# Kernel optimization log

Hardware: AMD Instinct MI355X
Metric: run time of the kernel (lower is better)

## Reference

```python
import jax, jax.numpy as jnp
import numpy as np

DIM = 1024
NUM_HEADS = 16
HEAD_DIM = 64
EPS = 1e-6

def setup_inputs() -> dict:
    key = jax.random.key(0)
    ks = jax.random.split(key, 6)
    x = jax.random.normal(ks[0], (4, 2048, DIM), dtype=jnp.float32)
    # Linear weights stored as (in, out); torch nn.Linear computes x @ W.T with W (out,in),
    # equivalent math with our (in,out) layout.
    Wq = jax.random.normal(ks[1], (DIM, NUM_HEADS * HEAD_DIM), dtype=jnp.float32) / np.sqrt(DIM)
    Wk = jax.random.normal(ks[2], (DIM, NUM_HEADS * HEAD_DIM), dtype=jnp.float32) / np.sqrt(DIM)
    Wv = jax.random.normal(ks[3], (DIM, NUM_HEADS * HEAD_DIM), dtype=jnp.float32) / np.sqrt(DIM)
    Wo = jax.random.normal(ks[4], (NUM_HEADS * HEAD_DIM, DIM), dtype=jnp.float32) / np.sqrt(NUM_HEADS * HEAD_DIM)
    # FeatureMap buffer: randn(head_dim, head_dim)/sqrt(head_dim)
    proj = jax.random.normal(ks[5], (HEAD_DIM, HEAD_DIM), dtype=jnp.float32) / np.sqrt(HEAD_DIM)
    return {"x": x, "Wq": Wq, "Wk": Wk, "Wv": Wv, "Wo": Wo, "proj": proj}

def _feature_map(x, proj):
    # phi(x) = elu(x @ proj) + 1  (positive features)
    return jax.nn.elu(x @ proj) + 1.0

def reference(x, Wq, Wk, Wv, Wo, proj):
    B, S, _ = x.shape
    H, D = NUM_HEADS, HEAD_DIM
    q = (x @ Wq).reshape(B, S, H, D)
    k = (x @ Wk).reshape(B, S, H, D)
    v = (x @ Wv).reshape(B, S, H, D)
    q = _feature_map(q, proj)
    k = _feature_map(k, proj)
    # scan over time: carry kv_state (B,H,D,D) and k_state (B,H,D)
    q_t = jnp.moveaxis(q, 1, 0)  # (S,B,H,D)
    k_t = jnp.moveaxis(k, 1, 0)
    v_t = jnp.moveaxis(v, 1, 0)

    def step(carry, qkv):
        kv, ksum = carry
        qt, kt, vt = qkv  # each (B,H,D)
        kv = kv + kt[..., :, None] * vt[..., None, :]  # outer product k v^T
        ksum = ksum + kt
        num = jnp.einsum('bhd,bhde->bhe', qt, kv)
        den = jnp.einsum('bhd,bhd->bh', qt, ksum) + EPS
        return (kv, ksum), num / den[..., None]

    kv0 = jnp.zeros((B, H, D, D), dtype=x.dtype)
    ks0 = jnp.zeros((B, H, D), dtype=x.dtype)
    _, out = jax.lax.scan(step, (kv0, ks0), (q_t, k_t, v_t))
    out = jnp.moveaxis(out, 0, 1).reshape(B, S, H * D)  # (B,S,H*D)
    return out @ Wo
```

## Files before the change

kernel.cpp:

```cpp
#include <hip/hip_runtime.h>

typedef unsigned short u16;
typedef unsigned int   u32;
typedef short bfrag8 __attribute__((ext_vector_type(8)));
typedef float facc4  __attribute__((ext_vector_type(4)));

#define DIM    1024
#define NH     16
#define HD     64
#define BSZ    4
#define SEQ    2048
#define MROWS  (BSZ*SEQ)
#define CHUNK  64
#define NCHUNK (SEQ/CHUNK)
#define BH     (BSZ*NH)
#define TS     72
#define NT32   32

__device__ __forceinline__ u16 f2bf(float f) {
  u32 u = __builtin_bit_cast(u32, f);
  u32 r = u + 0x7fffu + ((u >> 16) & 1u);
  return (u16)(r >> 16);
}
__device__ __forceinline__ float bf2f(u16 b) {
  return __builtin_bit_cast(float, (u32)b << 16);
}

__device__ __forceinline__ void gload_lds16(const void* g, void* l) {
  __builtin_amdgcn_global_load_lds((const __attribute__((address_space(1))) u32*)g,
                                   (__attribute__((address_space(3))) u32*)l, 16, 0, 0);
}


__global__ __launch_bounds__(256) void conv_f32_bf16(const float* __restrict__ in, u16* __restrict__ out) {
  const int i = (blockIdx.x * 256 + threadIdx.x) * 4;
  const float4 v = *(const float4*)(in + i);
  ushort4 o;
  o.x = f2bf(v.x); o.y = f2bf(v.y); o.z = f2bf(v.z); o.w = f2bf(v.w);
  *(ushort4*)(out + i) = o;
}

__global__ __launch_bounds__(256) void fold_qk(const float* __restrict__ Wq, const float* __restrict__ Wk,
                                               const float* __restrict__ proj, u16* __restrict__ wt) {
  const int i0 = blockIdx.x * 32;
  const int h  = blockIdx.y;
  const int sel = blockIdx.z;
  const float* W = sel ? Wk : Wq;
  u16* out = wt + (size_t)sel * (DIM*DIM);
  __shared__ float sp[64*64];
  __shared__ float sw[32*64];
  const int tid = threadIdx.x;
  for (int idx = tid; idx < 4096; idx += 256) sp[idx] = proj[idx];
  for (int idx = tid; idx < 2048; idx += 256) {
    int r = idx >> 6, c = idx & 63;
    sw[idx] = W[(size_t)(i0 + r)*DIM + h*64 + c];
  }
  __syncthreads();
  const int i  = tid >> 3;
  const int e0 = (tid & 7) * 8;
  #pragma unroll
  for (int ee = 0; ee < 8; ++ee) {
    const int e = e0 + ee;
    float acc = 0.f;
    for (int d = 0; d < 64; ++d) acc += sw[i*64 + d] * sp[d*64 + e];
    out[(size_t)(h*64 + e)*DIM + i0 + i] = f2bf(acc);
  }
}

__global__ __launch_bounds__(256) void trans_conv(const float* __restrict__ Wv, const float* __restrict__ Wo,
                                                  u16* __restrict__ wt) {
  const int sel = blockIdx.z;
  const float* in = sel ? Wo : Wv;
  u16* out = wt + (size_t)(2 + sel) * (DIM*DIM);
  const int n0 = blockIdx.x * 32, k0 = blockIdx.y * 32;
  __shared__ float tile[32][33];
  const int tid = threadIdx.x;
  for (int idx = tid; idx < 1024; idx += 256) {
    int r = idx >> 5, c = idx & 31;
    tile[r][c] = in[(size_t)(k0 + r)*DIM + n0 + c];
  }
  __syncthreads();
  for (int idx = tid; idx < 1024; idx += 256) {
    int r = idx >> 5, c = idx & 31;
    out[(size_t)(n0 + r)*DIM + k0 + c] = f2bf(tile[c][r]);
  }
}

template<int MODE>
__global__ __launch_bounds__(256, 3)
void gemm128(const u16* __restrict__ A, const u16* __restrict__ W,
             u16* __restrict__ outb, float* __restrict__ outf) {
  __shared__ u16 lds[2][2][4096];
  const int tid  = threadIdx.x;
  const int wave = tid >> 6, lane = tid & 63;
  const int wm = wave >> 1, wn = wave & 1;
  const int lr = lane & 15, g = lane >> 4;

  const int NY  = (MODE == 0) ? 24 : 8;
  const int q   = (int)gridDim.x >> 3;
  const int bid = (int)blockIdx.x;
  const int nf_ = (bid & 7) * q + (bid >> 3);
  const int m0  = (nf_ / NY) * 128;
  const int ngl = (nf_ % NY) * 128;

  auto stage = [&](int kt) {
    #pragma unroll
    for (int o = 0; o < 2; ++o) {
      const int L = o*256 + tid;
      const int row = L >> 2, s = L & 3;
      const int gc = ((s ^ ((row >> 1) & 3)) << 3);
      gload_lds16(A + (size_t)(m0  + row)*DIM + kt*32 + gc, &lds[kt & 1][0][(o*256 + wave*64)*8]);
      gload_lds16(W + (size_t)(ngl + row)*DIM + kt*32 + gc, &lds[kt & 1][1][(o*256 + wave*64)*8]);
    }
  };

  stage(0);
  __syncthreads();

  facc4 acc[4][4] = {};

  for (int t = 0; t < NT32; ++t) {
    if (t + 1 < NT32) stage(t + 1);
    const u16* lX = &lds[t & 1][0][0];
    const u16* lW = &lds[t & 1][1][0];
    bfrag8 xf[4], wf[4];
    #pragma unroll
    for (int mf = 0; mf < 4; ++mf) {
      const int row = wm*64 + mf*16 + lr;
      xf[mf] = *(const bfrag8*)&lX[row*32 + ((g ^ ((row >> 1) & 3)) << 3)];
    }
    #pragma unroll
    for (int nf = 0; nf < 4; ++nf) {
      const int row = wn*64 + nf*16 + lr;
      wf[nf] = *(const bfrag8*)&lW[row*32 + ((g ^ ((row >> 1) & 3)) << 3)];
    }
    __builtin_amdgcn_s_setprio(1);
    #pragma unroll
    for (int nf = 0; nf < 4; ++nf)
      #pragma unroll
      for (int mf = 0; mf < 4; ++mf)
        acc[nf][mf] = __builtin_amdgcn_mfma_f32_16x16x32_bf16(wf[nf], xf[mf], acc[nf][mf], 0, 0, 0);
    __builtin_amdgcn_s_setprio(0);
    __syncthreads();
  }

  const int sel = (MODE == 0) ? (ngl >> 10) : 0;
  const bool doElu = (MODE == 0) && (sel < 2);
  const int coly = (MODE == 0) ? (ngl & 1023) : ngl;
  #pragma unroll
  for (int nf = 0; nf < 4; ++nf) {
    #pragma unroll
    for (int mf = 0; mf < 4; ++mf) {
      const facc4 a = acc[nf][mf];
      const int m = m0 + wm*64 + mf*16 + lr;
      const int col0 = coly + wn*64 + nf*16 + g*4;
      float v0 = a[0], v1 = a[1], v2 = a[2], v3 = a[3];
      if (MODE == 0) {
        if (doElu) {
          v0 = (v0 > 0.f) ? (v0 + 1.f) : __expf(v0);
          v1 = (v1 > 0.f) ? (v1 + 1.f) : __expf(v1);
          v2 = (v2 > 0.f) ? (v2 + 1.f) : __expf(v2);
          v3 = (v3 > 0.f) ? (v3 + 1.f) : __expf(v3);
        }
        uint2 pk;
        pk.x = (u32)f2bf(v0) | ((u32)f2bf(v1) << 16);
        pk.y = (u32)f2bf(v2) | ((u32)f2bf(v3) << 16);
        *(uint2*)&outb[(size_t)sel*((size_t)MROWS*DIM) + (size_t)m*DIM + col0] = pk;
      } else {
        float4 pk; pk.x = v0; pk.y = v1; pk.z = v2; pk.w = v3;
        *(float4*)&outf[(size_t)m*DIM + col0] = pk;
      }
    }
  }
}


__global__ __launch_bounds__(256) void phaseA(const u16* __restrict__ Kb, const u16* __restrict__ Vb,
                                              u16* __restrict__ Ast, float* __restrict__ ksum) {
  const int c = blockIdx.x, bh = blockIdx.y;
  const int b = bh >> 4, h = bh & 15;
  const int tid = threadIdx.x;
  const int wave = tid >> 6, lane = tid & 63, lr = lane & 15, g = lane >> 4;
  __shared__ u16 lKt[64*TS];
  __shared__ u16 lVt[64*TS];
  const size_t mbase = (size_t)b*SEQ + (size_t)c*CHUNK;

  for (int s = tid; s < 512; s += 256) {
    const int t = s >> 3, dg = (s & 7) * 8;
    const bfrag8 kk = *(const bfrag8*)&Kb[(mbase + t)*DIM + h*64 + dg];
    const bfrag8 vv = *(const bfrag8*)&Vb[(mbase + t)*DIM + h*64 + dg];
    #pragma unroll
    for (int j = 0; j < 8; ++j) {
      lKt[(dg + j)*TS + t] = (u16)kk[j];
      lVt[(dg + j)*TS + t] = (u16)vv[j];
    }
  }
  __syncthreads();

  facc4 acc[4] = {};
  #pragma unroll
  for (int kt = 0; kt < 2; ++kt) {
    const bfrag8 af = *(const bfrag8*)&lVt[(wave*16 + lr)*TS + kt*32 + g*8];
    #pragma unroll
    for (int j = 0; j < 4; ++j) {
      const bfrag8 bk = *(const bfrag8*)&lKt[(j*16 + lr)*TS + kt*32 + g*8];
      acc[j] = __builtin_amdgcn_mfma_f32_16x16x32_bf16(af, bk, acc[j], 0, 0, 0);
    }
  }
  u16* dst = Ast + (((size_t)bh*NCHUNK + c) << 12);
  #pragma unroll
  for (int j = 0; j < 4; ++j)
    #pragma unroll
    for (int r = 0; r < 4; ++r)
      dst[(wave*16 + g*4 + r)*64 + j*16 + lr] = f2bf(acc[j][r]);

  const int d = tid >> 2, seg = tid & 3;
  const bfrag8 k0 = *(const bfrag8*)&lKt[d*TS + seg*16];
  const bfrag8 k1 = *(const bfrag8*)&lKt[d*TS + seg*16 + 8];
  float s = 0.f;
  #pragma unroll
  for (int j = 0; j < 8; ++j) s += bf2f((u16)k0[j]) + bf2f((u16)k1[j]);
  s += __shfl_xor(s, 1, 64);
  s += __shfl_xor(s, 2, 64);
  if (seg == 0) ksum[((size_t)bh*NCHUNK + c)*64 + d] = s;
}

__global__ __launch_bounds__(256) void phaseB(u16* __restrict__ Ast, float* __restrict__ ksum) {
  const int bh = blockIdx.x, slice = blockIdx.y;
  const int tid = threadIdx.x;
  u16* base = Ast + (size_t)bh*NCHUNK*4096 + slice*256 + tid;
  float v[NCHUNK];
  #pragma unroll
  for (int c = 0; c < NCHUNK; ++c) v[c] = bf2f(base[(size_t)c*4096]);
  float run = 0.f;
  #pragma unroll
  for (int c = 0; c < NCHUNK; ++c) { base[(size_t)c*4096] = f2bf(run); run += v[c]; }
  if (slice == 0 && tid < 64) {
    float rs = 0.f;
    float* kp = ksum + (size_t)bh*NCHUNK*64 + tid;
    for (int c = 0; c < NCHUNK; ++c) { const float t = kp[c*64]; kp[c*64] = rs; rs += t; }
  }
}

__global__ __launch_bounds__(256) void phaseC(const u16* __restrict__ Qb, const u16* __restrict__ Kb,
                                              const u16* __restrict__ Vb, const u16* __restrict__ Ast,
                                              const float* __restrict__ ksum, u16* __restrict__ Ob) {
  const int c = blockIdx.x, bh = blockIdx.y;
  const int b = bh >> 4, h = bh & 15;
  const int tid = threadIdx.x;
  const int wave = tid >> 6, lane = tid & 63, lr = lane & 15, g = lane >> 4;
  __shared__ u16 lS  [64*TS];
  __shared__ u16 lVt [64*TS];
  __shared__ u16 lKVt[64*TS];
  __shared__ float lks[64];
  __shared__ float lrs[64];
  __shared__ float lqk[64];
  const size_t mbase = (size_t)b*SEQ + (size_t)c*CHUNK;

  for (int s = tid; s < 512; s += 256) {
    const int t = s >> 3, dg = (s & 7) * 8;
    const bfrag8 vv = *(const bfrag8*)&Vb[(mbase + t)*DIM + h*64 + dg];
    #pragma unroll
    for (int j = 0; j < 8; ++j) lVt[(dg + j)*TS + t] = (u16)vv[j];
  }
  const u16* kvsrc = Ast + (((size_t)bh*NCHUNK + c) << 12);
  for (int s = tid; s < 512; s += 256) {
    const int e = s >> 3, dg = (s & 7) * 8;
    *(bfrag8*)&lKVt[e*TS + dg] = *(const bfrag8*)&kvsrc[e*64 + dg];
  }
  if (tid < 64) lks[tid] = ksum[((size_t)bh*NCHUNK + c)*64 + tid];

  bfrag8 qf[2], kf[4][2];
  {
    const u16* qrow = Qb + (mbase + wave*16 + lr)*DIM + h*64;
    qf[0] = *(const bfrag8*)&qrow[g*8];
    qf[1] = *(const bfrag8*)&qrow[32 + g*8];
  }
  #pragma unroll
  for (int j = 0; j < 4; ++j) {
    const u16* krow = Kb + (mbase + j*16 + lr)*DIM + h*64;
    kf[j][0] = *(const bfrag8*)&krow[g*8];
    kf[j][1] = *(const bfrag8*)&krow[32 + g*8];
  }

  facc4 accs[4] = {};
  #pragma unroll
  for (int kt = 0; kt < 2; ++kt)
    #pragma unroll
    for (int j = 0; j < 4; ++j)
      accs[j] = __builtin_amdgcn_mfma_f32_16x16x32_bf16(qf[kt], kf[j][kt], accs[j], 0, 0, 0);

  float rs[4] = {0.f, 0.f, 0.f, 0.f};
  #pragma unroll
  for (int j = 0; j < 4; ++j) {
    const int cc = j*16 + lr;
    #pragma unroll
    for (int r = 0; r < 4; ++r) {
      const int rr = wave*16 + g*4 + r;
      const float vS = (cc <= rr) ? accs[j][r] : 0.f;
      rs[r] += vS;
      lS[rr*TS + cc] = f2bf(vS);
    }
  }
  #pragma unroll
  for (int r = 0; r < 4; ++r) {
    float t = rs[r];
    t += __shfl_xor(t, 1, 64); t += __shfl_xor(t, 2, 64);
    t += __shfl_xor(t, 4, 64); t += __shfl_xor(t, 8, 64);
    if (lr == 0) lrs[wave*16 + g*4 + r] = t;
  }
  __syncthreads();

  {
    const u16* qr2 = Qb + (mbase + wave*16 + lr)*DIM + h*64 + g*16;
    const bfrag8 a0 = *(const bfrag8*)&qr2[0];
    const bfrag8 a1 = *(const bfrag8*)&qr2[8];
    float t = 0.f;
    #pragma unroll
    for (int j = 0; j < 8; ++j)
      t += bf2f((u16)a0[j]) * lks[g*16 + j] + bf2f((u16)a1[j]) * lks[g*16 + 8 + j];
    t += __shfl_xor(t, 16, 64);
    t += __shfl_xor(t, 32, 64);
    if (g == 0) lqk[wave*16 + lr] = t;
  }

  facc4 acco[4] = {};
  #pragma unroll
  for (int kt = 0; kt < 2; ++kt) {
    const bfrag8 sf = *(const bfrag8*)&lS[(wave*16 + lr)*TS + kt*32 + g*8];
    #pragma unroll
    for (int j = 0; j < 4; ++j) {
      const bfrag8 vf = *(const bfrag8*)&lVt[(j*16 + lr)*TS + kt*32 + g*8];
      acco[j] = __builtin_amdgcn_mfma_f32_16x16x32_bf16(sf, vf, acco[j], 0, 0, 0);
    }
  }
  #pragma unroll
  for (int kt = 0; kt < 2; ++kt)
    #pragma unroll
    for (int j = 0; j < 4; ++j) {
      const bfrag8 kvf = *(const bfrag8*)&lKVt[(j*16 + lr)*TS + kt*32 + g*8];
      acco[j] = __builtin_amdgcn_mfma_f32_16x16x32_bf16(qf[kt], kvf, acco[j], 0, 0, 0);
    }

  #pragma unroll
  for (int r = 0; r < 4; ++r) {
    const int rr = wave*16 + g*4 + r;
    const float rden = 1.0f / (lrs[rr] + lqk[rr] + 1e-6f);
    #pragma unroll
    for (int j = 0; j < 4; ++j)
      Ob[(mbase + rr)*DIM + h*64 + j*16 + lr] = f2bf(acco[j][r] * rden);
  }
}

extern "C" void kernel_launch(void* const* d_in, const int* in_sizes, int n_in,
                              void* d_out, int out_size, void* d_ws, size_t ws_size,
                              hipStream_t stream) {
  const float* x    = (const float*)d_in[0];
  const float* Wq   = (const float*)d_in[1];
  const float* Wk   = (const float*)d_in[2];
  const float* Wv   = (const float*)d_in[3];
  const float* Wo   = (const float*)d_in[4];
  const float* proj = (const float*)d_in[5];
  float* out = (float*)d_out;

  char* ws = (char*)d_ws;
  u16*   xb   = (u16*)  (ws);
  u16*   wt   = (u16*)  (ws + 16777216);
  u16*   qkv  = (u16*)  (ws + 25165824);
  u16*   Ob   = (u16*)  (ws + 75497472);
  u16*   Ast  = (u16*)  (ws + 92274688);
  float* ksum = (float*)(ws + 109051904);
  (void)ws_size; (void)in_sizes; (void)n_in; (void)out_size;

  conv_f32_bf16<<<dim3((MROWS*DIM)/1024), 256, 0, stream>>>(x, xb);
  fold_qk      <<<dim3(DIM/32, NH, 2), 256, 0, stream>>>(Wq, Wk, proj, wt);
  trans_conv   <<<dim3(DIM/32, DIM/32, 2), 256, 0, stream>>>(Wv, Wo, wt);

  gemm128<0><<<dim3(64*24), 256, 0, stream>>>(xb, wt, qkv, nullptr);

  const u16* Qb = qkv;
  const u16* Kb = qkv + (size_t)MROWS*DIM;
  const u16* Vb = qkv + 2*(size_t)MROWS*DIM;

  phaseA<<<dim3(NCHUNK, BH), 256, 0, stream>>>(Kb, Vb, Ast, ksum);
  phaseB<<<dim3(BH, 16), 256, 0, stream>>>(Ast, ksum);
  phaseC<<<dim3(NCHUNK, BH), 256, 0, stream>>>(Qb, Kb, Vb, Ast, ksum, Ob);

  gemm128<1><<<dim3(64*8), 256, 0, stream>>>(Ob, wt + 3*(size_t)DIM*DIM, nullptr, out);
}
```

Before: 192.7 us.

## Rewrite GEMMs as 128x256 tiles with triple-buffered LDS and phased MFMA schedule

Replaces the 128x128, 256-thread, double-buffered GEMM with a 512-thread kernel that computes 128x256 output tiles using a K-step of 64 and three LDS buffers. The loop is split into explicit phases, each with barriers, priority raises and vmcnt waits, so global-to-LDS loads for later K-steps interleave with MFMA clusters and fragment reads are register double-buffered. The aim is to raise data reuse per tile and hide load latency behind MFMA work. The cost is a large LDS footprint that allows one block per CU, fewer blocks for the output GEMM (256), and fragile hand-tuned waitcnt accounting.

```diff
diff --git a/kernel.cpp b/kernel.cpp
--- a/kernel.cpp
+++ b/kernel.cpp
@@ -15,7 +15,7 @@
 #define NCHUNK (SEQ/CHUNK)
 #define BH     (BSZ*NH)
 #define TS     72
-#define NT32   32
+#define NT     16
 
 __device__ __forceinline__ u16 f2bf(float f) {
   u32 u = __builtin_bit_cast(u32, f);
@@ -86,89 +86,149 @@
   }
 }
 
+
+#define PH_OPEN() { asm volatile("s_barrier" ::: "memory"); __builtin_amdgcn_sched_barrier(0); \
+                    __builtin_amdgcn_s_setprio(1); }
+#define PH_CLOSE(VM) { __builtin_amdgcn_s_setprio(0); __builtin_amdgcn_sched_barrier(0); \
+                       asm volatile("s_waitcnt vmcnt(" #VM ")" ::: "memory"); \
+                       asm volatile("s_barrier" ::: "memory"); }
+#define PH_CLOSE0() { __builtin_amdgcn_s_setprio(0); __builtin_amdgcn_sched_barrier(0); \
+                      asm volatile("s_barrier" ::: "memory"); }
+
+#define SU(mat, rb, kt, dstbase, seg) \
+  gload_lds16((mat) + (size_t)((rb) + (seg)*64 + (tid>>3))*DIM + (kt)*64 + ((((tid)&7) ^ ((tid>>3)&7)) << 3), \
+              (dstbase) + (seg)*4096 + tid*8);
+
+#define RDX01(dst, XB) { _Pragma("unroll") for(int mf=0;mf<2;++mf){ _Pragma("unroll") for(int kh=0;kh<2;++kh){ \
+  const int row = wm*64 + mf*16 + lr; \
+  dst[mf*2+kh] = *(const bfrag8*)&(XB)[row*64 + (((kh*4+g) ^ (row&7)) << 3)]; } } }
+#define RDX23(dst, XB) { _Pragma("unroll") for(int mf=0;mf<2;++mf){ _Pragma("unroll") for(int kh=0;kh<2;++kh){ \
+  const int row = wm*64 + (2+mf)*16 + lr; \
+  dst[mf*2+kh] = *(const bfrag8*)&(XB)[row*64 + (((kh*4+g) ^ (row&7)) << 3)]; } } }
+#define RDW01(dst, WB) { _Pragma("unroll") for(int nf=0;nf<2;++nf){ _Pragma("unroll") for(int kh=0;kh<2;++kh){ \
+  const int row = wn*32 + nf*16 + lr; \
+  dst[nf*2+kh] = *(const bfrag8*)&(WB)[row*64 + (((kh*4+g) ^ (row&7)) << 3)]; } } }
+#define RDW23(dst, WB) { _Pragma("unroll") for(int nf=0;nf<2;++nf){ _Pragma("unroll") for(int kh=0;kh<2;++kh){ \
+  const int row = 128 + wn*32 + nf*16 + lr; \
+  dst[nf*2+kh] = *(const bfrag8*)&(WB)[row*64 + (((kh*4+g) ^ (row&7)) << 3)]; } } }
+
+#define MMQ(NHh, MHh, XF, WF) { \
+  _Pragma("unroll") for(int nf=0;nf<2;++nf){ _Pragma("unroll") for(int mf=0;mf<2;++mf){ \
+  _Pragma("unroll") for(int kh=0;kh<2;++kh){ \
+    acc[(NHh)*2+nf][(MHh)*2+mf] = __builtin_amdgcn_mfma_f32_16x16x32_bf16( \
+        WF[nf*2+kh], XF[mf*2+kh], acc[(NHh)*2+nf][(MHh)*2+mf], 0, 0, 0); } } } }
+
 template<int MODE>
-__global__ __launch_bounds__(256, 3)
-void gemm128(const u16* __restrict__ A, const u16* __restrict__ W,
-             u16* __restrict__ outb, float* __restrict__ outf) {
-  __shared__ u16 lds[2][2][4096];
+__global__ __launch_bounds__(512, 1)
+void gemmR(const u16* __restrict__ A, const u16* __restrict__ W,
+           u16* __restrict__ outb, float* __restrict__ outf) {
+  __shared__ u16 lds[3*8192 + 3*16384];
+  u16* ldsX = lds;
+  u16* ldsW = lds + 3*8192;
   const int tid  = threadIdx.x;
   const int wave = tid >> 6, lane = tid & 63;
-  const int wm = wave >> 1, wn = wave & 1;
+  const int wm = wave >> 2, wn = wave & 3;
   const int lr = lane & 15, g = lane >> 4;
 
-  const int NY  = (MODE == 0) ? 24 : 8;
+  const int NY  = (MODE == 0) ? 12 : 4;
   const int q   = (int)gridDim.x >> 3;
   const int bid = (int)blockIdx.x;
   const int nf_ = (bid & 7) * q + (bid >> 3);
   const int m0  = (nf_ / NY) * 128;
-  const int ngl = (nf_ % NY) * 128;
-
-  auto stage = [&](int kt) {
-    #pragma unroll
-    for (int o = 0; o < 2; ++o) {
-      const int L = o*256 + tid;
-      const int row = L >> 2, s = L & 3;
-      const int gc = ((s ^ ((row >> 1) & 3)) << 3);
-      gload_lds16(A + (size_t)(m0  + row)*DIM + kt*32 + gc, &lds[kt & 1][0][(o*256 + wave*64)*8]);
-      gload_lds16(W + (size_t)(ngl + row)*DIM + kt*32 + gc, &lds[kt & 1][1][(o*256 + wave*64)*8]);
-    }
-  };
-
-  stage(0);
-  __syncthreads();
+  const int ngl = (nf_ % NY) * 256;
+
+  SU(A, m0, 0, ldsX, 0);            SU(A, m0, 0, ldsX, 1);
+  SU(W, ngl, 0, ldsW, 0);           SU(W, ngl, 0, ldsW, 1);
+  SU(W, ngl, 0, ldsW, 2);           SU(W, ngl, 0, ldsW, 3);
+  SU(A, m0, 1, ldsX + 8192, 0);     SU(A, m0, 1, ldsX + 8192, 1);
+  SU(W, ngl, 1, ldsW + 16384, 0);   SU(W, ngl, 1, ldsW + 16384, 1);
+  SU(W, ngl, 1, ldsW + 16384, 2);   SU(W, ngl, 1, ldsW + 16384, 3);
+  asm volatile("s_waitcnt vmcnt(6)" ::: "memory");
+  asm volatile("s_barrier" ::: "memory");
 
   facc4 acc[4][4] = {};
-
-  for (int t = 0; t < NT32; ++t) {
-    if (t + 1 < NT32) stage(t + 1);
-    const u16* lX = &lds[t & 1][0][0];
-    const u16* lW = &lds[t & 1][1][0];
-    bfrag8 xf[4], wf[4];
-    #pragma unroll
-    for (int mf = 0; mf < 4; ++mf) {
-      const int row = wm*64 + mf*16 + lr;
-      xf[mf] = *(const bfrag8*)&lX[row*32 + ((g ^ ((row >> 1) & 3)) << 3)];
-    }
-    #pragma unroll
-    for (int nf = 0; nf < 4; ++nf) {
-      const int row = wn*64 + nf*16 + lr;
-      wf[nf] = *(const bfrag8*)&lW[row*32 + ((g ^ ((row >> 1) & 3)) << 3)];
-    }
-    __builtin_amdgcn_s_setprio(1);
-    #pragma unroll
-    for (int nf = 0; nf < 4; ++nf)
-      #pragma unroll
-      for (int mf = 0; mf < 4; ++mf)
-        acc[nf][mf] = __builtin_amdgcn_mfma_f32_16x16x32_bf16(wf[nf], xf[mf], acc[nf][mf], 0, 0, 0);
+  bfrag8 xf01a[4], xf23a[4], wf01a[4], wf23a[4];
+  bfrag8 xf01b[4], xf23b[4], wf01b[4], wf23b[4];
+
+  RDX01(xf01a, ldsX); RDW01(wf01a, ldsW);
+
+  int bE = 0, bO = 1, bS = 2;
+  for (int p = 0; p < 7; ++p) {
+    const int E = 2*p;
+    const u16* xbE = ldsX + bE*8192;   u16* xbEm = ldsX + bE*8192;
+    const u16* wbE = ldsW + bE*16384;  u16* wbEm = ldsW + bE*16384;
+    const u16* xbO = ldsX + bO*8192;
+    const u16* wbO = ldsW + bO*16384;
+    u16* xbS = ldsX + bS*8192;
+    u16* wbS = ldsW + bS*16384;
+    RDX23(xf23a, xbE); SU(A, m0, E+2, xbS, 0); SU(A, m0, E+2, xbS, 1);
+    PH_OPEN(); MMQ(0,0,xf01a,wf01a); PH_CLOSE(8);
+    RDW23(wf23a, wbE); SU(W, ngl, E+2, wbS, 0); SU(W, ngl, E+2, wbS, 1);
+    PH_OPEN(); MMQ(0,1,xf23a,wf01a); PH_CLOSE(8);
+    RDX01(xf01b, xbO); SU(W, ngl, E+2, wbS, 2); SU(W, ngl, E+2, wbS, 3);
+    PH_OPEN(); MMQ(1,0,xf01a,wf23a); PH_CLOSE(8);
+    RDW01(wf01b, wbO);
+    PH_OPEN(); MMQ(1,1,xf23a,wf23a); PH_CLOSE0();
+    RDX23(xf23b, xbO); SU(A, m0, E+3, xbEm, 0); SU(A, m0, E+3, xbEm, 1);
+    PH_OPEN(); MMQ(0,0,xf01b,wf01b); PH_CLOSE(8);
+    RDW23(wf23b, wbO); SU(W, ngl, E+3, wbEm, 0); SU(W, ngl, E+3, wbEm, 1);
+    PH_OPEN(); MMQ(0,1,xf23b,wf01b); PH_CLOSE(8);
+    RDX01(xf01a, xbS); SU(W, ngl, E+3, wbEm, 2); SU(W, ngl, E+3, wbEm, 3);
+    PH_OPEN(); MMQ(1,0,xf01b,wf23b); PH_CLOSE(8);
+    RDW01(wf01a, wbS);
+    PH_OPEN(); MMQ(1,1,xf23b,wf23b); PH_CLOSE0();
+    const int t_ = bE; bE = bS; bS = bO; bO = t_;
+  }
+  {
+    const u16* xbE = ldsX + bE*8192;
+    const u16* wbE = ldsW + bE*16384;
+    const u16* xbO = ldsX + bO*8192;
+    const u16* wbO = ldsW + bO*16384;
+    RDX23(xf23a, xbE);
+    PH_OPEN(); MMQ(0,0,xf01a,wf01a); PH_CLOSE(6);
+    RDW23(wf23a, wbE);
+    PH_OPEN(); MMQ(0,1,xf23a,wf01a); PH_CLOSE(4);
+    RDX01(xf01b, xbO);
+    PH_OPEN(); MMQ(1,0,xf01a,wf23a); PH_CLOSE(2);
+    RDW01(wf01b, wbO);
+    PH_OPEN(); MMQ(1,1,xf23a,wf23a); PH_CLOSE0();
+    RDX23(xf23b, xbO);
+    PH_OPEN(); MMQ(0,0,xf01b,wf01b); PH_CLOSE(0);
+    RDW23(wf23b, wbO);
+    PH_OPEN(); MMQ(0,1,xf23b,wf01b); PH_CLOSE0();
+    PH_OPEN(); MMQ(1,0,xf01b,wf23b); PH_CLOSE0();
+    PH_OPEN(); MMQ(1,1,xf23b,wf23b);
     __builtin_amdgcn_s_setprio(0);
-    __syncthreads();
   }
 
   const int sel = (MODE == 0) ? (ngl >> 10) : 0;
   const bool doElu = (MODE == 0) && (sel < 2);
   const int coly = (MODE == 0) ? (ngl & 1023) : ngl;
   #pragma unroll
-  for (int nf = 0; nf < 4; ++nf) {
-    #pragma unroll
-    for (int mf = 0; mf < 4; ++mf) {
-      const facc4 a = acc[nf][mf];
-      const int m = m0 + wm*64 + mf*16 + lr;
-      const int col0 = coly + wn*64 + nf*16 + g*4;
-      float v0 = a[0], v1 = a[1], v2 = a[2], v3 = a[3];
-      if (MODE == 0) {
-        if (doElu) {
-          v0 = (v0 > 0.f) ? (v0 + 1.f) : __expf(v0);
-          v1 = (v1 > 0.f) ? (v1 + 1.f) : __expf(v1);
-          v2 = (v2 > 0.f) ? (v2 + 1.f) : __expf(v2);
-          v3 = (v3 > 0.f) ? (v3 + 1.f) : __expf(v3);
+  for (int nh = 0; nh < 2; ++nh) {
+    #pragma unroll
+    for (int nf = 0; nf < 2; ++nf) {
+      #pragma unroll
+      for (int mf = 0; mf < 4; ++mf) {
+        const facc4 a = acc[nh*2+nf][mf];
+        const int m = m0 + wm*64 + mf*16 + lr;
+        const int col0 = coly + nh*128 + wn*32 + nf*16 + g*4;
+        float v0 = a[0], v1 = a[1], v2 = a[2], v3 = a[3];
+        if (MODE == 0) {
+          if (doElu) {
+            v0 = (v0 > 0.f) ? (v0 + 1.f) : __expf(v0);
+            v1 = (v1 > 0.f) ? (v1 + 1.f) : __expf(v1);
+            v2 = (v2 > 0.f) ? (v2 + 1.f) : __expf(v2);
+            v3 = (v3 > 0.f) ? (v3 + 1.f) : __expf(v3);
+          }
+          uint2 pk;
+          pk.x = (u32)f2bf(v0) | ((u32)f2bf(v1) << 16);
+          pk.y = (u32)f2bf(v2) | ((u32)f2bf(v3) << 16);
+          *(uint2*)&outb[(size_t)sel*((size_t)MROWS*DIM) + (size_t)m*DIM + col0] = pk;
+        } else {
+          float4 pk; pk.x = v0; pk.y = v1; pk.z = v2; pk.w = v3;
+          *(float4*)&outf[(size_t)m*DIM + col0] = pk;
         }
-        uint2 pk;
-        pk.x = (u32)f2bf(v0) | ((u32)f2bf(v1) << 16);
-        pk.y = (u32)f2bf(v2) | ((u32)f2bf(v3) << 16);
-        *(uint2*)&outb[(size_t)sel*((size_t)MROWS*DIM) + (size_t)m*DIM + col0] = pk;
-      } else {
-        float4 pk; pk.x = v0; pk.y = v1; pk.z = v2; pk.w = v3;
-        *(float4*)&outf[(size_t)m*DIM + col0] = pk;
       }
     }
   }
@@ -376,7 +436,7 @@
   fold_qk      <<<dim3(DIM/32, NH, 2), 256, 0, stream>>>(Wq, Wk, proj, wt);
   trans_conv   <<<dim3(DIM/32, DIM/32, 2), 256, 0, stream>>>(Wv, Wo, wt);
 
-  gemm128<0><<<dim3(64*24), 256, 0, stream>>>(xb, wt, qkv, nullptr);
+  gemmR<0><<<dim3(64*12), 512, 0, stream>>>(xb, wt, qkv, nullptr);
 
   const u16* Qb = qkv;
   const u16* Kb = qkv + (size_t)MROWS*DIM;
@@ -386,5 +446,5 @@
   phaseB<<<dim3(BH, 16), 256, 0, stream>>>(Ast, ksum);
   phaseC<<<dim3(NCHUNK, BH), 256, 0, stream>>>(Qb, Kb, Vb, Ast, ksum, Ob);
 
-  gemm128<1><<<dim3(64*8), 256, 0, stream>>>(Ob, wt + 3*(size_t)DIM*DIM, nullptr, out);
-}
+  gemmR<1><<<dim3(64*4), 512, 0, stream>>>(Ob, wt + 3*(size_t)DIM*DIM, nullptr, out);
+}
```

Measured after the change: 189.5 us. Within noise of the previous version (-1.7%).

## Restructure projection GEMMs into 128x256 tiles with K=64 software-pipelined stages

Applied to the files above, without the earlier changes.

Replaces the 128x128, 256-thread GEMM with a 512-thread kernel that computes 128x256 output tiles. Each stage now covers K=64 using a new XOR swizzle, and the kernel prefetches two stages ahead with manual waitcnt, barriers and sched_barriers, splitting each stage into two half-K MFMA groups so LDS fragment reads overlap compute. The aim is more data reuse per tile, fewer barriers and better load/compute overlap. In exchange, only one block fits per CU and the output GEMM launches just 256 blocks, which may underfill the GPU. The hand-written waitcnt counts also carry correctness risk.

```diff
diff --git a/kernel.cpp b/kernel.cpp
--- a/kernel.cpp
+++ b/kernel.cpp
@@ -15,7 +15,7 @@
 #define NCHUNK (SEQ/CHUNK)
 #define BH     (BSZ*NH)
 #define TS     72
-#define NT32   32
+#define NT     16
 
 __device__ __forceinline__ u16 f2bf(float f) {
   u32 u = __builtin_bit_cast(u32, f);
@@ -86,62 +86,78 @@
   }
 }
 
+
+#define SBAR0() __builtin_amdgcn_sched_barrier(0)
+
+#define STAGE6(kt, bp) { \
+  const int rih = tid >> 3, sl = tid & 7; \
+  const int gc = ((sl ^ (rih & 7)) << 3); \
+  _Pragma("unroll") for (int seg = 0; seg < 2; ++seg) \
+    gload_lds16(A + (size_t)(m0 + seg*64 + rih)*DIM + (kt)*64 + gc, (bp) + seg*4096 + tid*8); \
+  _Pragma("unroll") for (int seg = 0; seg < 4; ++seg) \
+    gload_lds16(W + (size_t)(ngl + seg*64 + rih)*DIM + (kt)*64 + gc, (bp) + 8192 + seg*4096 + tid*8); \
+}
+
+#define RD8(xd, wd, bp, KH) { \
+  _Pragma("unroll") for (int mf = 0; mf < 4; ++mf) { \
+    const int row = wm*64 + mf*16 + lr; \
+    xd[mf] = *(const bfrag8*)&(bp)[row*64 + ((((KH)*4+g) ^ (row & 7)) << 3)]; } \
+  _Pragma("unroll") for (int nf = 0; nf < 4; ++nf) { \
+    const int row = wn*64 + nf*16 + lr; \
+    wd[nf] = *(const bfrag8*)&(bp)[8192 + row*64 + ((((KH)*4+g) ^ (row & 7)) << 3)]; } \
+}
+
+#define MM16(xs, ws) { __builtin_amdgcn_s_setprio(1); \
+  _Pragma("unroll") for (int nf = 0; nf < 4; ++nf) \
+    _Pragma("unroll") for (int mf = 0; mf < 4; ++mf) \
+      acc[nf][mf] = __builtin_amdgcn_mfma_f32_16x16x32_bf16(ws[nf], xs[mf], acc[nf][mf], 0, 0, 0); \
+  __builtin_amdgcn_s_setprio(0); }
+
 template<int MODE>
-__global__ __launch_bounds__(256, 3)
-void gemm128(const u16* __restrict__ A, const u16* __restrict__ W,
-             u16* __restrict__ outb, float* __restrict__ outf) {
-  __shared__ u16 lds[2][2][4096];
+__global__ __launch_bounds__(512, 1)
+void gemmK(const u16* __restrict__ A, const u16* __restrict__ W,
+           u16* __restrict__ outb, float* __restrict__ outf) {
+  __shared__ u16 lds[2*24576];
   const int tid  = threadIdx.x;
   const int wave = tid >> 6, lane = tid & 63;
-  const int wm = wave >> 1, wn = wave & 1;
+  const int wm = wave >> 2, wn = wave & 3;
   const int lr = lane & 15, g = lane >> 4;
 
-  const int NY  = (MODE == 0) ? 24 : 8;
+  const int NY  = (MODE == 0) ? 12 : 4;
   const int q   = (int)gridDim.x >> 3;
   const int bid = (int)blockIdx.x;
   const int nf_ = (bid & 7) * q + (bid >> 3);
   const int m0  = (nf_ / NY) * 128;
-  const int ngl = (nf_ % NY) * 128;
-
-  auto stage = [&](int kt) {
-    #pragma unroll
-    for (int o = 0; o < 2; ++o) {
-      const int L = o*256 + tid;
-      const int row = L >> 2, s = L & 3;
-      const int gc = ((s ^ ((row >> 1) & 3)) << 3);
-      gload_lds16(A + (size_t)(m0  + row)*DIM + kt*32 + gc, &lds[kt & 1][0][(o*256 + wave*64)*8]);
-      gload_lds16(W + (size_t)(ngl + row)*DIM + kt*32 + gc, &lds[kt & 1][1][(o*256 + wave*64)*8]);
-    }
-  };
-
-  stage(0);
-  __syncthreads();
+  const int ngl = (nf_ % NY) * 256;
+
+  STAGE6(0, lds);
+  STAGE6(1, lds + 24576);
+  asm volatile("s_waitcnt vmcnt(6)" ::: "memory");
+  asm volatile("s_barrier" ::: "memory");
 
   facc4 acc[4][4] = {};
-
-  for (int t = 0; t < NT32; ++t) {
-    if (t + 1 < NT32) stage(t + 1);
-    const u16* lX = &lds[t & 1][0][0];
-    const u16* lW = &lds[t & 1][1][0];
-    bfrag8 xf[4], wf[4];
-    #pragma unroll
-    for (int mf = 0; mf < 4; ++mf) {
-      const int row = wm*64 + mf*16 + lr;
-      xf[mf] = *(const bfrag8*)&lX[row*32 + ((g ^ ((row >> 1) & 3)) << 3)];
-    }
-    #pragma unroll
-    for (int nf = 0; nf < 4; ++nf) {
-      const int row = wn*64 + nf*16 + lr;
-      wf[nf] = *(const bfrag8*)&lW[row*32 + ((g ^ ((row >> 1) & 3)) << 3)];
-    }
-    __builtin_amdgcn_s_setprio(1);
-    #pragma unroll
-    for (int nf = 0; nf < 4; ++nf)
-      #pragma unroll
-      for (int mf = 0; mf < 4; ++mf)
-        acc[nf][mf] = __builtin_amdgcn_mfma_f32_16x16x32_bf16(wf[nf], xf[mf], acc[nf][mf], 0, 0, 0);
-    __builtin_amdgcn_s_setprio(0);
-    __syncthreads();
+  bfrag8 xa[4], wa[4], xb[4], wb[4];
+
+  RD8(xa, wa, lds, 0);
+
+  #pragma unroll 2
+  for (int t = 0; t < NT; ++t) {
+    u16* bufp = lds + (t & 1) * 24576;
+    u16* bufq = lds + ((t + 1) & 1) * 24576;
+    asm volatile("s_waitcnt lgkmcnt(0)" ::: "memory"); SBAR0();
+    RD8(xb, wb, bufp, 1);
+    SBAR0();
+    MM16(xa, wa);
+    SBAR0();
+    asm volatile("s_waitcnt vmcnt(0)" ::: "memory");
+    asm volatile("s_barrier" ::: "memory");
+    asm volatile("s_waitcnt lgkmcnt(0)" ::: "memory"); SBAR0();
+    if (t + 2 < NT) STAGE6(t + 2, bufp);
+    if (t + 1 < NT) RD8(xa, wa, bufq, 0);
+    SBAR0();
+    MM16(xb, wb);
+    SBAR0();
+    asm volatile("s_barrier" ::: "memory");
   }
 
   const int sel = (MODE == 0) ? (ngl >> 10) : 0;
@@ -376,7 +392,7 @@
   fold_qk      <<<dim3(DIM/32, NH, 2), 256, 0, stream>>>(Wq, Wk, proj, wt);
   trans_conv   <<<dim3(DIM/32, DIM/32, 2), 256, 0, stream>>>(Wv, Wo, wt);
 
-  gemm128<0><<<dim3(64*24), 256, 0, stream>>>(xb, wt, qkv, nullptr);
+  gemmK<0><<<dim3(64*12), 512, 0, stream>>>(xb, wt, qkv, nullptr);
 
   const u16* Qb = qkv;
   const u16* Kb = qkv + (size_t)MROWS*DIM;
@@ -386,5 +402,5 @@
   phaseB<<<dim3(BH, 16), 256, 0, stream>>>(Ast, ksum);
   phaseC<<<dim3(NCHUNK, BH), 256, 0, stream>>>(Qb, Kb, Vb, Ast, ksum, Ob);
 
-  gemm128<1><<<dim3(64*8), 256, 0, stream>>>(Ob, wt + 3*(size_t)DIM*DIM, nullptr, out);
-}
+  gemmK<1><<<dim3(64*4), 512, 0, stream>>>(Ob, wt + 3*(size_t)DIM*DIM, nullptr, out);
+}
```

Result: faster. 186.6 us (-3.1%).
